# Optimization experiments

Measured on AMD Instinct MI355X. Metric: run time of the kernel, lower is better.

The kernel has to match this reference:

```python
import jax, jax.numpy as jnp
import numpy as np

HEIGHT, WIDTH = 300, 25
ROI_COLS = (3, 8, 12, 14, 17, 19)

def _roi_map():
    m = np.zeros((1, HEIGHT, WIDTH), dtype=np.float32)
    m[0, :, list(ROI_COLS)] = 1.0
    return jnp.asarray(m)

def _l2_normalize(x, axis, eps=1e-12):
    # matches keras.backend.l2_normalize: x / sqrt(max(sum(x^2), eps))
    sq = jnp.sum(jnp.square(x), axis=axis, keepdims=True)
    return x * jax.lax.rsqrt(jnp.maximum(sq, eps))

def setup_inputs() -> dict:
    key = jax.random.key(0)
    k1, k2, k3 = jax.random.split(key, 3)
    B, C = 1024, 16
    return {
        "s_o": jax.random.normal(k1, (B, WIDTH), dtype=jnp.float32),
        "t_o": jax.random.normal(k2, (B, HEIGHT), dtype=jnp.float32),
        "ipt": jax.random.normal(k3, (B, HEIGHT, WIDTH, C), dtype=jnp.float32),
    }

def reference(s_o, t_o, ipt):
    roi = _roi_map()                              # [1, 300, 25]
    s = _l2_normalize(s_o, axis=1)                # [B, 25]
    t = _l2_normalize(t_o, axis=1)                # [B, 300]
    # outer product via broadcasting (original tiles with 300+25 concats)
    a = t[:, :, None] * s[:, None, :] + roi       # [B, 300, 25]
    return a[:, :, :, None] * ipt                 # [B, 300, 25, C]
```

## Files before the change

kernel.cpp:

```cpp
#include <hip/hip_runtime.h>
#include <math.h>

#define HEIGHT 300
#define WIDTH  25
#define CH     16
#define BATCH  1024
#define ROI_MASK 0x000A5108u

__global__ void __launch_bounds__(64)
norms_kernel(const float* __restrict__ s_o,
             const float* __restrict__ t_o,
             float* __restrict__ inv) {
    const int b = blockIdx.x;
    const int lane = threadIdx.x;

    float acc_t = 0.f;
    const float* tr = t_o + b * HEIGHT;
    for (int i = lane; i < HEIGHT; i += 64) {
        float v = tr[i];
        acc_t += v * v;
    }
    float acc_s = 0.f;
    if (lane < WIDTH) {
        float v = s_o[b * WIDTH + lane];
        acc_s = v * v;
    }
    #pragma unroll
    for (int off = 32; off > 0; off >>= 1) {
        acc_t += __shfl_down(acc_t, off, 64);
        acc_s += __shfl_down(acc_s, off, 64);
    }
    if (lane == 0) {
        inv[b]         = 1.0f / sqrtf(fmaxf(acc_t, 1e-12f));
        inv[BATCH + b] = 1.0f / sqrtf(fmaxf(acc_s, 1e-12f));
    }
}

__global__ void __launch_bounds__(256)
scale_kernel(const float* __restrict__ s_o,
             const float* __restrict__ t_o,
             const float4* __restrict__ ipt,
             const float* __restrict__ inv,
             float4* __restrict__ out) {
    const int n4 = BATCH * HEIGHT * WIDTH * (CH / 4);
    int i = blockIdx.x * blockDim.x + threadIdx.x;
    if (i >= n4) return;

    int p  = i >> 2;
    int w  = p % WIDTH;
    int bh = p / WIDTH;
    int h  = bh % HEIGHT;
    int b  = bh / HEIGHT;

    float roi = (float)((ROI_MASK >> w) & 1u);
    float a = (t_o[b * HEIGHT + h] * inv[b]) * (s_o[b * WIDTH + w] * inv[BATCH + b]) + roi;

    float4 v = ipt[i];
    float4 o;
    o.x = v.x * a;
    o.y = v.y * a;
    o.z = v.z * a;
    o.w = v.w * a;
    out[i] = o;
}

extern "C" void kernel_launch(void* const* d_in, const int* in_sizes, int n_in,
                              void* d_out, int out_size, void* d_ws, size_t ws_size,
                              hipStream_t stream) {
    const float* s_o = (const float*)d_in[0];
    const float* t_o = (const float*)d_in[1];
    const float* ipt = (const float*)d_in[2];
    float* out = (float*)d_out;
    float* inv = (float*)d_ws;

    norms_kernel<<<BATCH, 64, 0, stream>>>(s_o, t_o, inv);

    const int n4 = BATCH * HEIGHT * WIDTH * (CH / 4);
    const int blocks = (n4 + 255) / 256;
    scale_kernel<<<blocks, 256, 0, stream>>>(s_o, t_o, (const float4*)ipt, inv,
                                             (float4*)out);
}
```

Baseline: 751.7 us.

## Precompute full attention map then stream input with nontemporal grid-stride kernel

Adds a first kernel that normalizes s and t per batch and writes the full 300x25 scale map (with ROI) to workspace. A second grid-stride kernel with a fixed grid then reads one map value per float4, loading the input and storing the output with nontemporal hints. The goal is to remove the per-element integer div/mod index math and the scattered gathers of t_o, s_o and inv from the main streaming kernel. The cost is about 30MB of extra map traffic and a dependence on workspace size, with a fallback to the old path when the workspace is too small.

```diff
diff --git a/kernel.cpp b/kernel.cpp
--- a/kernel.cpp
+++ b/kernel.cpp
@@ -7,13 +7,82 @@
 #define BATCH  1024
 #define ROI_MASK 0x000A5108u
 
+#define NCELL (BATCH * HEIGHT * WIDTH)
+#define N4    (NCELL * (CH / 4))
+
+typedef float f4_t __attribute__((ext_vector_type(4)));
+
+__global__ void __launch_bounds__(64)
+amap_kernel(const float* __restrict__ s_o,
+            const float* __restrict__ t_o,
+            float* __restrict__ amap) {
+    __shared__ float t_lds[HEIGHT];
+    __shared__ float s_lds[WIDTH];
+    const int b    = blockIdx.x;
+    const int lane = threadIdx.x;
+
+    const float* tr = t_o + b * HEIGHT;
+    float tv[5];
+    float acc_t = 0.f;
+    #pragma unroll
+    for (int k = 0; k < 5; ++k) {
+        int i = lane + 64 * k;
+        tv[k] = (i < HEIGHT) ? tr[i] : 0.f;
+        acc_t += tv[k] * tv[k];
+    }
+    float sv = (lane < WIDTH) ? s_o[b * WIDTH + lane] : 0.f;
+    float acc_s = sv * sv;
+
+    #pragma unroll
+    for (int off = 32; off > 0; off >>= 1) {
+        acc_t += __shfl_down(acc_t, off, 64);
+        acc_s += __shfl_down(acc_s, off, 64);
+    }
+    float sum_t = __shfl(acc_t, 0, 64);
+    float sum_s = __shfl(acc_s, 0, 64);
+    float inv_t = 1.0f / sqrtf(fmaxf(sum_t, 1e-12f));
+    float inv_s = 1.0f / sqrtf(fmaxf(sum_s, 1e-12f));
+
+    #pragma unroll
+    for (int k = 0; k < 5; ++k) {
+        int i = lane + 64 * k;
+        if (i < HEIGHT) t_lds[i] = tv[k] * inv_t;
+    }
+    if (lane < WIDTH) s_lds[lane] = sv * inv_s;
+    __syncthreads();
+
+    float* am = amap + b * (HEIGHT * WIDTH);
+    for (int idx = lane; idx < HEIGHT * WIDTH; idx += 64) {
+        int h = (int)((unsigned)idx / WIDTH);
+        int w = idx - h * WIDTH;
+        float roi = (float)((ROI_MASK >> w) & 1u);
+        am[idx] = fmaf(t_lds[h], s_lds[w], roi);
+    }
+}
+
+__global__ void __launch_bounds__(256)
+apply_kernel(const f4_t* __restrict__ ipt,
+             const float* __restrict__ amap,
+             f4_t* __restrict__ out) {
+    const int stride = gridDim.x * 256;
+    for (int i = blockIdx.x * 256 + threadIdx.x; i < N4; i += stride) {
+        float a = amap[i >> 2];
+        f4_t v  = __builtin_nontemporal_load(ipt + i);
+        f4_t o;
+        o.x = v.x * a;
+        o.y = v.y * a;
+        o.z = v.z * a;
+        o.w = v.w * a;
+        __builtin_nontemporal_store(o, out + i);
+    }
+}
+
 __global__ void __launch_bounds__(64)
 norms_kernel(const float* __restrict__ s_o,
              const float* __restrict__ t_o,
              float* __restrict__ inv) {
     const int b = blockIdx.x;
     const int lane = threadIdx.x;
-
     float acc_t = 0.f;
     const float* tr = t_o + b * HEIGHT;
     for (int i = lane; i < HEIGHT; i += 64) {
@@ -42,19 +111,16 @@
              const float4* __restrict__ ipt,
              const float* __restrict__ inv,
              float4* __restrict__ out) {
-    const int n4 = BATCH * HEIGHT * WIDTH * (CH / 4);
+    const int n4 = N4;
     int i = blockIdx.x * blockDim.x + threadIdx.x;
     if (i >= n4) return;
-
     int p  = i >> 2;
     int w  = p % WIDTH;
     int bh = p / WIDTH;
     int h  = bh % HEIGHT;
     int b  = bh / HEIGHT;
-
     float roi = (float)((ROI_MASK >> w) & 1u);
     float a = (t_o[b * HEIGHT + h] * inv[b]) * (s_o[b * WIDTH + w] * inv[BATCH + b]) + roi;
-
     float4 v = ipt[i];
     float4 o;
     o.x = v.x * a;
@@ -71,12 +137,16 @@
     const float* t_o = (const float*)d_in[1];
     const float* ipt = (const float*)d_in[2];
     float* out = (float*)d_out;
-    float* inv = (float*)d_ws;
 
-    norms_kernel<<<BATCH, 64, 0, stream>>>(s_o, t_o, inv);
-
-    const int n4 = BATCH * HEIGHT * WIDTH * (CH / 4);
-    const int blocks = (n4 + 255) / 256;
-    scale_kernel<<<blocks, 256, 0, stream>>>(s_o, t_o, (const float4*)ipt, inv,
-                                             (float4*)out);
+    if (ws_size >= (size_t)NCELL * sizeof(float)) {
+        float* amap = (float*)d_ws;
+        amap_kernel<<<BATCH, 64, 0, stream>>>(s_o, t_o, amap);
+        apply_kernel<<<2048, 256, 0, stream>>>((const f4_t*)ipt, amap, (f4_t*)out);
+    } else {
+        float* inv = (float*)d_ws;
+        norms_kernel<<<BATCH, 64, 0, stream>>>(s_o, t_o, inv);
+        const int blocks = (N4 + 255) / 256;
+        scale_kernel<<<blocks, 256, 0, stream>>>(s_o, t_o, (const float4*)ipt, inv,
+                                                 (float4*)out);
+    }
 }
```

Result: slower. 784.4 us (+4.3%).
